# Kernel optimization log

Measured on AMD Instinct MI355X. Metric: run time of the kernel, lower is better.

The kernel has to match this reference:

```python
import jax, jax.numpy as jnp
import numpy as np

H = 768      # hidden_size (MambaConfig default)
DI = 500     # intermediate_size (overridden)
N = 16       # state_size
R = 48       # time_step_rank = ceil(768/16)
K = 4        # conv_kernel
LYR = 5      # num_hidden_layers
EPS = 1e-5   # layer_norm_epsilon
B, L, IN = 8, 1024, 4096


def _rmsnorm(x, w):
    v = jnp.mean(jnp.square(x), axis=-1, keepdims=True)
    return x * jax.lax.rsqrt(v + EPS) * w


def _mixer(x, in_proj, conv_w, conv_b, x_proj, dt_w, dt_b, A_log, Dp, out_w):
    # x: [B, L, H]
    proj = x @ in_proj                       # [B, L, 2*DI]
    u, gate = jnp.split(proj, 2, axis=-1)
    # causal depthwise conv1d (torch Conv1d padding=K-1, sliced to L)
    up = jnp.pad(u, ((0, 0), (K - 1, 0), (0, 0)))
    conv = conv_b
    for k in range(K):
        conv = conv + up[:, k:k + x.shape[1], :] * conv_w[:, k]
    u = jax.nn.silu(conv)                    # [B, L, DI]
    ssm = u @ x_proj                         # [B, L, R + 2N]
    dt, Bm, Cm = ssm[..., :R], ssm[..., R:R + N], ssm[..., R + N:]
    dt = jax.nn.softplus(dt @ dt_w + dt_b)   # [B, L, DI]
    A = -jnp.exp(A_log)                      # [DI, N]
    dA = jnp.exp(dt[..., None] * A)          # [B, L, DI, N]
    dBu = dt[..., None] * Bm[:, :, None, :] * u[..., None]  # [B, L, DI, N]

    def step(h, xs):
        dA_t, dBu_t, C_t = xs
        h = dA_t * h + dBu_t                 # [B, DI, N]
        y = jnp.einsum('bdn,bn->bd', h, C_t)
        return h, y

    h0 = jnp.zeros((u.shape[0], DI, N), dtype=u.dtype)
    _, ys = jax.lax.scan(step, h0, (dA.transpose(1, 0, 2, 3),
                                    dBu.transpose(1, 0, 2, 3),
                                    Cm.transpose(1, 0, 2)))
    y = ys.transpose(1, 0, 2)                # [B, L, DI]
    y = y + u * Dp
    y = y * jax.nn.silu(gate)
    return y @ out_w                         # [B, L, H]


def setup_inputs() -> dict:
    key = jax.random.key(0)
    ks = jax.random.split(key, 12)
    s = 0.02
    inputs = jax.random.normal(ks[0], (B, L, IN), jnp.float32)
    W_down = jax.random.normal(ks[1], (IN, H), jnp.float32) * s
    in_proj = jax.random.normal(ks[2], (LYR, H, 2 * DI), jnp.float32) * s
    conv_w = jax.random.normal(ks[3], (LYR, DI, K), jnp.float32) * 0.1
    conv_b = jnp.zeros((LYR, DI), jnp.float32)
    x_proj = jax.random.normal(ks[4], (LYR, DI, R + 2 * N), jnp.float32) * s
    dt_w = jax.random.normal(ks[5], (LYR, R, DI), jnp.float32) * s
    dt_b = jax.random.normal(ks[6], (LYR, DI), jnp.float32) * 0.1
    A_log = jnp.broadcast_to(jnp.log(jnp.arange(1, N + 1, dtype=jnp.float32)),
                             (LYR, DI, N)).copy()
    D_param = jnp.ones((LYR, DI), jnp.float32)
    out_w = jax.random.normal(ks[7], (LYR, DI, H), jnp.float32) * s
    norm_w = jnp.ones((LYR, H), jnp.float32)
    norm_f_w = jnp.ones((H,), jnp.float32)
    W_cls = jax.random.normal(ks[8], (H, 1), jnp.float32) * s
    return dict(inputs=inputs, W_down=W_down, in_proj=in_proj, conv_w=conv_w,
                conv_b=conv_b, x_proj=x_proj, dt_w=dt_w, dt_b=dt_b,
                A_log=A_log, D_param=D_param, out_w=out_w, norm_w=norm_w,
                norm_f_w=norm_f_w, W_cls=W_cls)


def reference(inputs, W_down, in_proj, conv_w, conv_b, x_proj, dt_w, dt_b,
              A_log, D_param, out_w, norm_w, norm_f_w, W_cls):
    x = inputs @ W_down                      # down projection [B, L, H]
    for i in range(LYR):
        x = x + _mixer(_rmsnorm(x, norm_w[i]), in_proj[i], conv_w[i],
                       conv_b[i], x_proj[i], dt_w[i], dt_b[i], A_log[i],
                       D_param[i], out_w[i])
    x = _rmsnorm(x, norm_f_w)
    out = x[:, -1]                           # last token [B, H]
    logits = out @ W_cls                     # [B, 1]
    return logits
```

## Files before the change

kernel.cpp:

```cpp
#include <hip/hip_runtime.h>
#include <hip/hip_bf16.h>

#define BATCH 8
#define SEQL 1024
#define INDIM 4096
#define HDIM 768
#define DI 500
#define NSTATE 16
#define RRANK 48
#define KCONV 4
#define NLAYER 5
#define BL (BATCH * SEQL)

typedef __attribute__((ext_vector_type(8))) short bf16x8;
typedef __attribute__((ext_vector_type(4))) float f32x4;

__device__ __forceinline__ void gl_lds16(const void* g, void* l) {
  __builtin_amdgcn_global_load_lds(
      (const __attribute__((address_space(1))) void*)g,
      (__attribute__((address_space(3))) void*)l, 16, 0, 0);
}

__device__ __forceinline__ unsigned short f2bf(float v) {
  return __hip_bfloat16_raw(__float2bfloat16(v)).x;
}
__device__ __forceinline__ float bf2f(unsigned short h) {
  unsigned int u = ((unsigned int)h) << 16;
  float f;
  memcpy(&f, &u, 4);
  return f;
}

template <int CTRL>
__device__ __forceinline__ float ror_add(float x) {
  int r = __builtin_amdgcn_update_dpp(0, __float_as_int(x), CTRL, 0xf, 0xf,
                                      true);
  return x + __int_as_float(r);
}

template <int EPI>
__global__ __launch_bounds__(256) void gemm_mfma(
    const short* __restrict__ A, const short* __restrict__ Bt,
    float* __restrict__ C, const float* __restrict__ bias,
    unsigned short* __restrict__ D0, unsigned short* __restrict__ D1,
    int M, int N, int K, int lda, int ldb, int ldc) {
  __shared__ short As[3][128 * 32];
  __shared__ short Bs[3][128 * 32];
  const int tid = threadIdx.x;
  const int w = tid >> 6, lane = tid & 63;

  const int gx = gridDim.x;
  const int nwg = gx * gridDim.y;
  int flat = blockIdx.y * gx + blockIdx.x;
  flat = (flat & 7) * (nwg >> 3) + (flat >> 3);
  const int m0 = (flat / gx) * 128, n0 = (flat % gx) * 128;

  const int wr = (w >> 1), wc = w & 1;
  f32x4 acc[4][4] = {};

  const int srow = tid >> 2;
  const int cpos = tid & 3;
  const int sc = (cpos ^ ((srow >> 1) & 3)) * 8;
  const short* ga0 = A + (size_t)(m0 + srow) * lda + sc;
  const short* ga1 = A + (size_t)(m0 + 64 + srow) * lda + sc;
  const short* gb0 = Bt + (size_t)(n0 + srow) * ldb + sc;
  const short* gb1 = Bt + (size_t)(n0 + 64 + srow) * ldb + sc;
  const int lr = lane & 15, kb = lane >> 4;
  const int kbx = (kb ^ ((lr >> 1) & 3)) * 8;

  auto stage = [&](int buf, int k0) {
    gl_lds16(ga0 + k0, &As[buf][w * 512]);
    gl_lds16(ga1 + k0, &As[buf][2048 + w * 512]);
    gl_lds16(gb0 + k0, &Bs[buf][w * 512]);
    gl_lds16(gb1 + k0, &Bs[buf][2048 + w * 512]);
  };
  auto compute = [&](int buf) {
    bf16x8 af[4], bfr[4];
#pragma unroll
    for (int i = 0; i < 4; ++i) {
      af[i] = *(const bf16x8*)&As[buf][(wr * 64 + i * 16 + lr) * 32 + kbx];
      bfr[i] = *(const bf16x8*)&Bs[buf][(wc * 64 + i * 16 + lr) * 32 + kbx];
    }
#pragma unroll
    for (int i = 0; i < 4; ++i)
#pragma unroll
      for (int j = 0; j < 4; ++j)
        acc[i][j] = __builtin_amdgcn_mfma_f32_16x16x32_bf16(af[i], bfr[j],
                                                            acc[i][j], 0, 0, 0);
  };

  const int nk = K >> 5;
  stage(0, 0);
  if (nk > 1) stage(1, 32);
  int cur = 0;
  for (int t = 0; t < nk; ++t) {
    if (t + 1 < nk)
      asm volatile("s_waitcnt vmcnt(4)" ::: "memory");
    else
      asm volatile("s_waitcnt vmcnt(0)" ::: "memory");
    __builtin_amdgcn_s_barrier();
    __builtin_amdgcn_sched_barrier(0);
    compute(cur);
    if (t + 2 < nk) {
      int nb = cur + 2;
      if (nb >= 3) nb -= 3;
      stage(nb, (t + 2) * 32);
    }
    ++cur;
    if (cur == 3) cur = 0;
  }

#pragma unroll
  for (int i = 0; i < 4; ++i) {
    const int row = m0 + wr * 64 + i * 16 + (lane >> 4) * 4;
#pragma unroll
    for (int j = 0; j < 4; ++j) {
      const int col = n0 + wc * 64 + j * 16 + (lane & 15);
      if (EPI == 3) {
        if (col < N) {
          float4 v4;
#pragma unroll
          for (int r = 0; r < 4; ++r) {
            float v = acc[i][j][r] + bias[col];
            ((float*)&v4)[r] = (v > 15.f) ? v : log1pf(expf(v));
          }
          const int bb = row >> 10, tt = row & 1023;
          *(float4*)&C[((size_t)bb * DI + col) * 1024 + tt] = v4;
        }
      } else if (EPI == 4) {
#pragma unroll
        for (int r = 0; r < 4; ++r) {
          unsigned short h = f2bf(acc[i][j][r]);
          size_t rr = (size_t)(row + r);
          if (col < DI)
            D0[rr * 512 + col] = h;
          else
            D1[rr * 512 + (col - DI)] = h;
        }
      } else if (EPI == 5) {
#pragma unroll
        for (int r = 0; r < 4; ++r) {
          float v = acc[i][j][r];
          size_t rr = (size_t)(row + r);
          if (col < 64) D0[rr * 64 + col] = f2bf(col < RRANK ? v : 0.f);
          if (col >= RRANK && col < 64) C[rr * 32 + 2 * (col - RRANK)] = v;
          if (col >= 64 && col < 80) C[rr * 32 + 2 * (col - 64) + 1] = v;
        }
      } else {
        if (col < N) {
#pragma unroll
          for (int r = 0; r < 4; ++r) {
            float v = acc[i][j][r];
            size_t idx = (size_t)(row + r) * ldc + col;
            if (EPI == 1) v += C[idx];
            C[idx] = v;
          }
        }
      }
    }
  }
}

__global__ __launch_bounds__(256) void convert_cast(
    const float* __restrict__ src, __hip_bfloat16* __restrict__ dst, long n) {
  long i = ((long)blockIdx.x * 256 + threadIdx.x) * 4;
  if (i >= n) return;
  float4 v = *(const float4*)(src + i);
  dst[i + 0] = __float2bfloat16(v.x);
  dst[i + 1] = __float2bfloat16(v.y);
  dst[i + 2] = __float2bfloat16(v.z);
  dst[i + 3] = __float2bfloat16(v.w);
}

__global__ __launch_bounds__(256) void convert_wT(
    const float* __restrict__ src, __hip_bfloat16* __restrict__ dst, int K,
    int N, int Kpad, int Npad, long src_lstride, long dst_lstride) {
  int idx = blockIdx.x * 256 + threadIdx.x;
  int per = Kpad * Npad;
  if (idx >= per) return;
  const float* s = src + (long)blockIdx.y * src_lstride;
  __hip_bfloat16* d = dst + (long)blockIdx.y * dst_lstride;
  int n = idx / Kpad, k = idx % Kpad;
  float v = (k < K && n < N) ? s[(long)k * N + n] : 0.f;
  d[idx] = __float2bfloat16(v);
}

__device__ __forceinline__ float block_sum256(float v, float* sm) {
#pragma unroll
  for (int off = 32; off > 0; off >>= 1) v += __shfl_down(v, off, 64);
  int wid = threadIdx.x >> 6;
  if ((threadIdx.x & 63) == 0) sm[wid] = v;
  __syncthreads();
  float t = sm[0] + sm[1] + sm[2] + sm[3];
  __syncthreads();
  return t;
}

__global__ __launch_bounds__(256) void rmsnorm_kernel(
    const float* __restrict__ X, const float* __restrict__ w,
    __hip_bfloat16* __restrict__ XN) {
  __shared__ float sm[4];
  const long row = blockIdx.x;
  const float* x = X + row * HDIM;
  float vals[3];
  float s = 0.f;
#pragma unroll
  for (int j = 0; j < 3; ++j) {
    vals[j] = x[threadIdx.x + j * 256];
    s += vals[j] * vals[j];
  }
  float tot = block_sum256(s, sm);
  float scale = rsqrtf(tot / (float)HDIM + 1e-5f);
#pragma unroll
  for (int j = 0; j < 3; ++j) {
    int c = threadIdx.x + j * 256;
    XN[row * HDIM + c] = __float2bfloat16(vals[j] * scale * w[c]);
  }
}

__global__ __launch_bounds__(256) void conv_fused_kernel(
    const unsigned short* __restrict__ Uraw, const float* __restrict__ cw,
    const float* __restrict__ cb, unsigned short* __restrict__ Ubf,
    unsigned short* __restrict__ Ut, int layer) {
  __shared__ unsigned short tin[35][33];
  __shared__ unsigned short tout[32][33];
  const int d0 = blockIdx.x * 32, t0 = blockIdx.y * 32, b = blockIdx.z;
  const int tx = threadIdx.x & 31, ty = threadIdx.x >> 5;
#pragma unroll
  for (int r = 0; r < 5; ++r) {
    int tr = ty + r * 8;
    if (tr < 35) {
      int t = t0 + tr - (KCONV - 1);
      tin[tr][tx] =
          (t >= 0) ? Uraw[((size_t)b * 1024 + t) * 512 + d0 + tx] : 0;
    }
  }
  __syncthreads();
  const int d = d0 + tx;
  float w0 = 0.f, w1 = 0.f, w2 = 0.f, w3 = 0.f, bias = 0.f;
  if (d < DI) {
    const float* w = cw + ((size_t)layer * DI + d) * KCONV;
    w0 = w[0]; w1 = w[1]; w2 = w[2]; w3 = w[3];
    bias = cb[layer * DI + d];
  }
#pragma unroll
  for (int r = 0; r < 4; ++r) {
    const int tt = ty + r * 8;
    unsigned short h = 0;
    if (d < DI) {
      float a = bias + w0 * bf2f(tin[tt][tx]) + w1 * bf2f(tin[tt + 1][tx]) +
                w2 * bf2f(tin[tt + 2][tx]) + w3 * bf2f(tin[tt + 3][tx]);
      h = f2bf(a / (1.f + expf(-a)));
    }
    tout[tt][tx] = h;
    Ubf[((size_t)b * 1024 + t0 + tt) * 512 + d] = h;
  }
  __syncthreads();
#pragma unroll
  for (int r = 0; r < 4; ++r) {
    const int dd = ty + r * 8;
    Ut[((size_t)b * 512 + d0 + dd) * 1024 + t0 + tx] = tout[tx][dd];
  }
}

__global__ __launch_bounds__(256) void y_gate_kernel(
    const unsigned short* __restrict__ Yt, const unsigned short* __restrict__ G,
    unsigned short* __restrict__ Ybf) {
  __shared__ unsigned short tile[32][33];
  const int d0 = blockIdx.x * 32, t0 = blockIdx.y * 32, b = blockIdx.z;
  const int tx = threadIdx.x & 31, ty = threadIdx.x >> 5;
#pragma unroll
  for (int r = 0; r < 4; ++r) {
    int d = d0 + ty + r * 8;
    tile[ty + r * 8][tx] =
        (d < DI) ? Yt[((size_t)b * 512 + d) * 1024 + t0 + tx]
                 : (unsigned short)0;
  }
  __syncthreads();
#pragma unroll
  for (int r = 0; r < 4; ++r) {
    size_t row = (size_t)b * 1024 + t0 + ty + r * 8;
    int d = d0 + tx;
    float yv = 0.f;
    if (d < DI) {
      float y = bf2f(tile[tx][ty + r * 8]);
      float g = bf2f(G[row * 512 + d]);
      yv = y * (g / (1.f + expf(-g)));
    }
    Ybf[row * 512 + d] = f2bf(yv);
  }
}

__global__ __launch_bounds__(256) void scan_kernel(
    const float* __restrict__ DTt, const unsigned short* __restrict__ Ut,
    const float* __restrict__ BC, const float* __restrict__ A_log,
    const float* __restrict__ Dparam, unsigned short* __restrict__ Yt,
    int layer) {
  __shared__ float2 sdtu[2][1036];
  __shared__ float s_ap[8][2][16];
  __shared__ float s_h0[8][2][16];
  __shared__ float s_hi[8][2][16];
  const int orig = blockIdx.x;
  const int blk = (orig & 7) * 250 + (orig >> 3);
  const int b = blk / 250;
  const int d0 = (blk - b * 250) * 2;
  const int tid = threadIdx.x;
  const int c = tid >> 5;
  const int dl = (tid >> 4) & 1;
  const int n = tid & 15;
  const int d = d0 + dl;

#pragma unroll
  for (int k = 0; k < 8; ++k) {
    int x = tid + k * 256;
    int dd = x >> 10, t = x & 1023;
    float dtv = DTt[((size_t)b * DI + d0 + dd) * 1024 + t];
    float uv = bf2f(Ut[((size_t)b * 512 + d0 + dd) * 1024 + t]);
    sdtu[dd][t] = make_float2(dtv, uv);
  }
  __syncthreads();

  const float An2 =
      -expf(A_log[((size_t)layer * DI + d) * NSTATE + n]) * 1.44269504f;
  const float Dp = Dparam[layer * DI + d];
  const int t0 = c * 128;
  const float2* sb = &sdtu[dl][t0];
  const float2* bcp = (const float2*)(BC + ((size_t)b * 1024 + t0) * 32) + n;

  {
    float h = 0.f, cum = 0.f;
#pragma unroll 8
    for (int s = 0; s < 128; ++s) {
      float2 du = sb[s];
      float a = exp2f(du.x * An2);
      cum += du.x;
      h = a * h + du.x * du.y * bcp[s * 16].x;
    }
    s_ap[c][dl][n] = exp2f(An2 * cum);
    s_h0[c][dl][n] = h;
  }
  __syncthreads();

  if (tid < 32) {
    float hi = 0.f;
    for (int cc = 0; cc < 8; ++cc) {
      s_hi[cc][dl][n] = hi;
      hi = s_ap[cc][dl][n] * hi + s_h0[cc][dl][n];
    }
  }
  __syncthreads();

  {
    float h = s_hi[c][dl][n];
    unsigned short* yp = Yt + ((size_t)b * 512 + d) * 1024 + t0;
#pragma unroll 4
    for (int s = 0; s < 128; s += 2) {
      float2 du0 = sb[s], du1 = sb[s + 1];
      float2 v0 = bcp[s * 16], v1 = bcp[(s + 1) * 16];
      float a0 = exp2f(du0.x * An2);
      h = a0 * h + du0.x * du0.y * v0.x;
      float p0 = h * v0.y;
      float a1 = exp2f(du1.x * An2);
      h = a1 * h + du1.x * du1.y * v1.x;
      float p1 = h * v1.y;
      p0 = ror_add<0x128>(p0);
      p1 = ror_add<0x128>(p1);
      p0 = ror_add<0x124>(p0);
      p1 = ror_add<0x124>(p1);
      p0 = ror_add<0x122>(p0);
      p1 = ror_add<0x122>(p1);
      p0 = ror_add<0x121>(p0);
      p1 = ror_add<0x121>(p1);
      if (n == 0) {
        float y0 = p0 + du0.y * Dp;
        float y1 = p1 + du1.y * Dp;
        unsigned int pk =
            (unsigned int)f2bf(y0) | ((unsigned int)f2bf(y1) << 16);
        *(unsigned int*)(yp + s) = pk;
      }
    }
  }
}

__global__ __launch_bounds__(256) void final_kernel(
    const float* __restrict__ X, const float* __restrict__ nfw,
    const float* __restrict__ Wcls, float* __restrict__ out) {
  __shared__ float sm[4];
  const int b = blockIdx.x;
  const long row = (long)b * SEQL + (SEQL - 1);
  const float* x = X + row * HDIM;
  float vals[3];
  float s = 0.f;
#pragma unroll
  for (int j = 0; j < 3; ++j) {
    vals[j] = x[threadIdx.x + j * 256];
    s += vals[j] * vals[j];
  }
  float tot = block_sum256(s, sm);
  float scale = rsqrtf(tot / (float)HDIM + 1e-5f);
  float dot = 0.f;
#pragma unroll
  for (int j = 0; j < 3; ++j) {
    int c = threadIdx.x + j * 256;
    dot += vals[j] * scale * nfw[c] * Wcls[c];
  }
  float td = block_sum256(dot, sm);
  if (threadIdx.x == 0) out[b] = td;
}

extern "C" void kernel_launch(void* const* d_in, const int* in_sizes, int n_in,
                              void* d_out, int out_size, void* d_ws,
                              size_t ws_size, hipStream_t stream) {
  const float* inputs  = (const float*)d_in[0];
  const float* W_down  = (const float*)d_in[1];
  const float* in_proj = (const float*)d_in[2];
  const float* conv_w  = (const float*)d_in[3];
  const float* conv_b  = (const float*)d_in[4];
  const float* x_proj  = (const float*)d_in[5];
  const float* dt_w    = (const float*)d_in[6];
  const float* dt_b    = (const float*)d_in[7];
  const float* A_log   = (const float*)d_in[8];
  const float* D_param = (const float*)d_in[9];
  const float* out_w   = (const float*)d_in[10];
  const float* norm_w  = (const float*)d_in[11];
  const float* norm_fw = (const float*)d_in[12];
  const float* W_cls   = (const float*)d_in[13];
  float* out = (float*)d_out;

  char* ws = (char*)d_ws;
  __hip_bfloat16* Abf   = (__hip_bfloat16*)(ws + 0);
  __hip_bfloat16* Wdbf  = (__hip_bfloat16*)(ws + 67108864);
  __hip_bfloat16* XNbf  = (__hip_bfloat16*)(ws + 0);
  unsigned short* Yt    = (unsigned short*)(ws + 0);
  float*          DTt   = (float*)(ws + 12582912);
  unsigned short* Uraw  = (unsigned short*)(ws + 28966912);
  unsigned short* Ybf   = (unsigned short*)(ws + 28966912);
  unsigned short* Gate  = (unsigned short*)(ws + 37355520);
  unsigned short* Ubf   = (unsigned short*)(ws + 45744128);
  unsigned short* Ut    = (unsigned short*)(ws + 54132736);
  float*          BC    = (float*)(ws + 62521344);
  __hip_bfloat16* SSMbf = (__hip_bfloat16*)(ws + 66715648);
  float*          X     = (float*)(ws + 73400320);
  __hip_bfloat16* inpbf = (__hip_bfloat16*)(ws + 98566144);
  __hip_bfloat16* xpbf  = (__hip_bfloat16*)(ws + 106430464);
  __hip_bfloat16* dtwbf = (__hip_bfloat16*)(ws + 107085824);
  __hip_bfloat16* outwbf= (__hip_bfloat16*)(ws + 107413504);

  convert_cast<<<(long)BL * 4096 / 4 / 256, 256, 0, stream>>>(inputs, Abf,
                                                              (long)BL * 4096);
  convert_wT<<<dim3((768 * 4096 + 255) / 256, 1), 256, 0, stream>>>(
      W_down, Wdbf, 4096, 768, 4096, 768, 0, 0);
  convert_wT<<<dim3((768 * 1024 + 255) / 256, NLAYER), 256, 0, stream>>>(
      in_proj, inpbf, 768, 1000, 768, 1024, (long)HDIM * 1000, 768 * 1024);
  convert_wT<<<dim3((128 * 512 + 255) / 256, NLAYER), 256, 0, stream>>>(
      x_proj, xpbf, 500, 80, 512, 128, (long)DI * 80, 128 * 512);
  convert_wT<<<dim3((512 * 64 + 255) / 256, NLAYER), 256, 0, stream>>>(
      dt_w, dtwbf, 48, 500, 64, 512, (long)RRANK * DI, 512 * 64);
  convert_wT<<<dim3((768 * 512 + 255) / 256, NLAYER), 256, 0, stream>>>(
      out_w, outwbf, 500, 768, 512, 768, (long)DI * HDIM, 768 * 512);

  gemm_mfma<0><<<dim3(768 / 128, BL / 128), 256, 0, stream>>>(
      (const short*)Abf, (const short*)Wdbf, X, nullptr, nullptr, nullptr, BL,
      HDIM, INDIM, INDIM, INDIM, HDIM);

  for (int i = 0; i < NLAYER; ++i) {
    rmsnorm_kernel<<<BL, 256, 0, stream>>>(X, norm_w + i * HDIM, XNbf);
    gemm_mfma<4><<<dim3(1024 / 128, BL / 128), 256, 0, stream>>>(
        (const short*)XNbf, (const short*)(inpbf + (long)i * 768 * 1024),
        nullptr, nullptr, Uraw, Gate, BL, 1000, HDIM, HDIM, HDIM, 0);
    conv_fused_kernel<<<dim3(16, 32, 8), 256, 0, stream>>>(Uraw, conv_w,
                                                           conv_b, Ubf, Ut, i);
    gemm_mfma<5><<<dim3(1, BL / 128), 256, 0, stream>>>(
        (const short*)Ubf, (const short*)(xpbf + (long)i * 128 * 512), BC,
        nullptr, (unsigned short*)SSMbf, nullptr, BL, 80, 512, 512, 512, 0);
    gemm_mfma<3><<<dim3(512 / 128, BL / 128), 256, 0, stream>>>(
        (const short*)SSMbf, (const short*)(dtwbf + (long)i * 512 * 64), DTt,
        dt_b + i * DI, nullptr, nullptr, BL, DI, 64, 64, 64, 0);
    scan_kernel<<<2000, 256, 0, stream>>>(DTt, Ut, BC, A_log, D_param, Yt, i);
    y_gate_kernel<<<dim3(16, 32, 8), 256, 0, stream>>>(Yt, Gate, Ybf);
    gemm_mfma<1><<<dim3(768 / 128, BL / 128), 256, 0, stream>>>(
        (const short*)Ybf, (const short*)(outwbf + (long)i * 768 * 512), X,
        nullptr, nullptr, nullptr, BL, HDIM, 512, 512, 512, HDIM);
  }

  final_kernel<<<BATCH, 256, 0, stream>>>(X, norm_fw, W_cls, out);
}
```

Measured before the change: 1.128 ms.

## Fuse SiLU gate into scan and store gate transposed from in_proj GEMM

The in_proj GEMM epilogue now writes the gate half in a time-major transposed layout [B, DI, L] using packed 64-bit stores, so the scan kernel can read the gate contiguously alongside its output. The scan applies y * silu(gate) before storing, and y_gate_kernel becomes a pure transpose with no gate read or activation math. This is meant to remove a separate strided gate read and the elementwise work from the transpose pass. In exchange it adds exp work and a gate load on the scan's lane-0 path, and it relies on the padded columns 500..511 of Ybf being zero from the zero-filled tile.

Result: slower. 1.303 ms (+15.6%).

```diff
diff --git a/kernel.cpp b/kernel.cpp
--- a/kernel.cpp
+++ b/kernel.cpp
@@ -128,14 +128,18 @@
           *(float4*)&C[((size_t)bb * DI + col) * 1024 + tt] = v4;
         }
       } else if (EPI == 4) {
-#pragma unroll
-        for (int r = 0; r < 4; ++r) {
-          unsigned short h = f2bf(acc[i][j][r]);
-          size_t rr = (size_t)(row + r);
-          if (col < DI)
-            D0[rr * 512 + col] = h;
-          else
-            D1[rr * 512 + (col - DI)] = h;
+        if (col < DI) {
+#pragma unroll
+          for (int r = 0; r < 4; ++r)
+            D0[(size_t)(row + r) * 512 + col] = f2bf(acc[i][j][r]);
+        } else if (col < 1000) {
+          unsigned long long pk = 0;
+#pragma unroll
+          for (int r = 0; r < 4; ++r)
+            pk |= (unsigned long long)f2bf(acc[i][j][r]) << (16 * r);
+          const int bb = row >> 10, tt = row & 1023;
+          *(unsigned long long*)&D1[((size_t)bb * 512 + (col - DI)) * 1024 +
+                                    tt] = pk;
         }
       } else if (EPI == 5) {
 #pragma unroll
@@ -264,8 +268,7 @@
 }
 
 __global__ __launch_bounds__(256) void y_gate_kernel(
-    const unsigned short* __restrict__ Yt, const unsigned short* __restrict__ G,
-    unsigned short* __restrict__ Ybf) {
+    const unsigned short* __restrict__ Yt, unsigned short* __restrict__ Ybf) {
   __shared__ unsigned short tile[32][33];
   const int d0 = blockIdx.x * 32, t0 = blockIdx.y * 32, b = blockIdx.z;
   const int tx = threadIdx.x & 31, ty = threadIdx.x >> 5;
@@ -280,22 +283,15 @@
 #pragma unroll
   for (int r = 0; r < 4; ++r) {
     size_t row = (size_t)b * 1024 + t0 + ty + r * 8;
-    int d = d0 + tx;
-    float yv = 0.f;
-    if (d < DI) {
-      float y = bf2f(tile[tx][ty + r * 8]);
-      float g = bf2f(G[row * 512 + d]);
-      yv = y * (g / (1.f + expf(-g)));
-    }
-    Ybf[row * 512 + d] = f2bf(yv);
+    Ybf[row * 512 + d0 + tx] = tile[tx][ty + r * 8];
   }
 }
 
 __global__ __launch_bounds__(256) void scan_kernel(
     const float* __restrict__ DTt, const unsigned short* __restrict__ Ut,
-    const float* __restrict__ BC, const float* __restrict__ A_log,
-    const float* __restrict__ Dparam, unsigned short* __restrict__ Yt,
-    int layer) {
+    const float* __restrict__ BC, const unsigned short* __restrict__ Gt,
+    const float* __restrict__ A_log, const float* __restrict__ Dparam,
+    unsigned short* __restrict__ Yt, int layer) {
   __shared__ float2 sdtu[2][1036];
   __shared__ float s_ap[8][2][16];
   __shared__ float s_h0[8][2][16];
@@ -352,6 +348,7 @@
 
   {
     float h = s_hi[c][dl][n];
+    const unsigned short* gp = Gt + ((size_t)b * 512 + d) * 1024 + t0;
     unsigned short* yp = Yt + ((size_t)b * 512 + d) * 1024 + t0;
 #pragma unroll 4
     for (int s = 0; s < 128; s += 2) {
@@ -372,8 +369,11 @@
       p0 = ror_add<0x121>(p0);
       p1 = ror_add<0x121>(p1);
       if (n == 0) {
-        float y0 = p0 + du0.y * Dp;
-        float y1 = p1 + du1.y * Dp;
+        unsigned int gpk = *(const unsigned int*)(gp + s);
+        float g0 = bf2f((unsigned short)(gpk & 0xffff));
+        float g1 = bf2f((unsigned short)(gpk >> 16));
+        float y0 = (p0 + du0.y * Dp) * (g0 / (1.f + expf(-g0)));
+        float y1 = (p1 + du1.y * Dp) * (g1 / (1.f + expf(-g1)));
         unsigned int pk =
             (unsigned int)f2bf(y0) | ((unsigned int)f2bf(y1) << 16);
         *(unsigned int*)(yp + s) = pk;
@@ -435,7 +435,7 @@
   float*          DTt   = (float*)(ws + 12582912);
   unsigned short* Uraw  = (unsigned short*)(ws + 28966912);
   unsigned short* Ybf   = (unsigned short*)(ws + 28966912);
-  unsigned short* Gate  = (unsigned short*)(ws + 37355520);
+  unsigned short* Gt    = (unsigned short*)(ws + 37355520);
   unsigned short* Ubf   = (unsigned short*)(ws + 45744128);
   unsigned short* Ut    = (unsigned short*)(ws + 54132736);
   float*          BC    = (float*)(ws + 62521344);
@@ -467,7 +467,7 @@
     rmsnorm_kernel<<<BL, 256, 0, stream>>>(X, norm_w + i * HDIM, XNbf);
     gemm_mfma<4><<<dim3(1024 / 128, BL / 128), 256, 0, stream>>>(
         (const short*)XNbf, (const short*)(inpbf + (long)i * 768 * 1024),
-        nullptr, nullptr, Uraw, Gate, BL, 1000, HDIM, HDIM, HDIM, 0);
+        nullptr, nullptr, Uraw, Gt, BL, 1000, HDIM, HDIM, HDIM, 0);
     conv_fused_kernel<<<dim3(16, 32, 8), 256, 0, stream>>>(Uraw, conv_w,
                                                            conv_b, Ubf, Ut, i);
     gemm_mfma<5><<<dim3(1, BL / 128), 256, 0, stream>>>(
@@ -476,8 +476,9 @@
     gemm_mfma<3><<<dim3(512 / 128, BL / 128), 256, 0, stream>>>(
         (const short*)SSMbf, (const short*)(dtwbf + (long)i * 512 * 64), DTt,
         dt_b + i * DI, nullptr, nullptr, BL, DI, 64, 64, 64, 0);
-    scan_kernel<<<2000, 256, 0, stream>>>(DTt, Ut, BC, A_log, D_param, Yt, i);
-    y_gate_kernel<<<dim3(16, 32, 8), 256, 0, stream>>>(Yt, Gate, Ybf);
+    scan_kernel<<<2000, 256, 0, stream>>>(DTt, Ut, BC, Gt, A_log, D_param, Yt,
+                                          i);
+    y_gate_kernel<<<dim3(16, 32, 8), 256, 0, stream>>>(Yt, Ybf);
     gemm_mfma<1><<<dim3(768 / 128, BL / 128), 256, 0, stream>>>(
         (const short*)Ybf, (const short*)(outwbf + (long)i * 768 * 512), X,
         nullptr, nullptr, nullptr, BL, HDIM, 512, 512, 512, HDIM);
```
